# Kernel optimization log

Hardware: AMD Instinct MI355X
Metric: run time of the kernel (lower is better)

The kernel has to match this reference:

```python
import jax, jax.numpy as jnp
import numpy as np

V, T_BLOCK, E, H, L = 65, 256, 384, 6, 10
HS = E // H  # 64


def _ln(x, scale, bias, eps=1e-5):
    mu = jnp.mean(x, axis=-1, keepdims=True)
    var = jnp.mean(jnp.square(x - mu), axis=-1, keepdims=True)
    return (x - mu) * jax.lax.rsqrt(var + eps) * scale + bias


def setup_inputs() -> dict:
    key = jax.random.key(0)
    ks = jax.random.split(key, 20)
    B, T = 64, 256
    s = 0.02
    return {
        "encoding": jax.random.randint(ks[0], (B, T), 0, V),
        "tok_emb": jax.random.normal(ks[1], (V, E), jnp.float32) * s,
        "pos_emb": jax.random.normal(ks[2], (T_BLOCK, E), jnp.float32) * s,
        "Wq": jax.random.normal(ks[3], (L, H, E, HS), jnp.float32) * s,
        "Wk": jax.random.normal(ks[4], (L, H, E, HS), jnp.float32) * s,
        "Wv": jax.random.normal(ks[5], (L, H, E, HS), jnp.float32) * s,
        "Wo": jax.random.normal(ks[6], (L, E, E), jnp.float32) * s,
        "bo": jnp.zeros((L, E), jnp.float32),
        "W1": jax.random.normal(ks[7], (L, E, 4 * E), jnp.float32) * s,
        "b1": jnp.zeros((L, 4 * E), jnp.float32),
        "W2": jax.random.normal(ks[8], (L, 4 * E, E), jnp.float32) * s,
        "b2": jnp.zeros((L, E), jnp.float32),
        "ln1_s": jnp.ones((L, E), jnp.float32),
        "ln1_b": jnp.zeros((L, E), jnp.float32),
        "ln2_s": jnp.ones((L, E), jnp.float32),
        "ln2_b": jnp.zeros((L, E), jnp.float32),
        "lnf_s": jnp.ones((E,), jnp.float32),
        "lnf_b": jnp.zeros((E,), jnp.float32),
        "Wout": jax.random.normal(ks[9], (E, V), jnp.float32) * s,
        "bout": jnp.zeros((V,), jnp.float32),
    }


def reference(encoding, tok_emb, pos_emb, Wq, Wk, Wv, Wo, bo, W1, b1, W2, b2,
              ln1_s, ln1_b, ln2_s, ln2_b, lnf_s, lnf_b, Wout, bout):
    B, T = encoding.shape
    x = tok_emb[encoding] + pos_emb[:T]  # [B,T,E]
    causal = jnp.tril(jnp.ones((T, T), bool))
    scale = jnp.asarray(E, x.dtype) ** -0.5  # NOTE: original scales by embeddingSize, not headSize
    for l in range(L):
        h = _ln(x, ln1_s[l], ln1_b[l])
        q = jnp.einsum('bte,hed->bhtd', h, Wq[l])
        k = jnp.einsum('bte,hed->bhtd', h, Wk[l])
        v = jnp.einsum('bte,hed->bhtd', h, Wv[l])
        scores = jnp.einsum('bhtd,bhsd->bhts', q, k) * scale
        scores = jnp.where(causal, scores, -jnp.inf)
        w = jax.nn.softmax(scores, axis=-1)  # dropout inactive (eval)
        attn = jnp.einsum('bhts,bhsd->bhtd', w, v)  # [B,H,T,HS]
        attn = attn.transpose(0, 2, 1, 3).reshape(B, T, E)  # concat heads
        x = x + attn @ Wo[l] + bo[l]
        h2 = _ln(x, ln2_s[l], ln2_b[l])
        x = x + jax.nn.relu(h2 @ W1[l] + b1[l]) @ W2[l] + b2[l]
    x = _ln(x, lnf_s, lnf_b)
    logits = x @ Wout + bout  # [B,T,V]
    return logits
```

## Files before the change

kernel.cpp:

```cpp
#include <hip/hip_runtime.h>

typedef __bf16 bf16;
typedef __bf16 bf16x4 __attribute__((ext_vector_type(4)));
typedef __bf16 bf16x8 __attribute__((ext_vector_type(8)));
typedef float floatx4 __attribute__((ext_vector_type(4)));

#define NB   64
#define NT   256
#define NE   384
#define NH   6
#define NHS  64
#define NL   10
#define NTOK (NB*NT)
#define NFF  1536
#define NQKV 1152
#define NV   65
#define NVP  128

#define ATTN_SCALE 0.051031036307982884f

__device__ __forceinline__ void glds16(const bf16* g, bf16* l)
{
    __builtin_amdgcn_global_load_lds(
        (const __attribute__((address_space(1))) void*)g,
        (__attribute__((address_space(3))) void*)l, 16, 0, 0);
}

template<int K, int N>
__global__ __launch_bounds__(256) void pack_mat_t(const float* __restrict__ src, bf16* __restrict__ dst)
{
    __shared__ float tile[64][65];
    const int n0 = blockIdx.x * 64, k0 = blockIdx.y * 64, l = blockIdx.z;
    const int tid = threadIdx.x;
    const float* sp = src + (size_t)l * K * N;
#pragma unroll
    for (int it = 0; it < 4; ++it) {
        int kl = (tid >> 4) + it * 16;
        int nl = (tid & 15) * 4;
        float4 v = *(const float4*)(sp + (size_t)(k0 + kl) * N + n0 + nl);
        tile[kl][nl] = v.x; tile[kl][nl + 1] = v.y; tile[kl][nl + 2] = v.z; tile[kl][nl + 3] = v.w;
    }
    __syncthreads();
#pragma unroll
    for (int it = 0; it < 2; ++it) {
        int chunk = it * 256 + tid;
        int nl = chunk >> 3, kc = chunk & 7;
        bf16x8 o;
#pragma unroll
        for (int j = 0; j < 8; ++j) o[j] = (bf16)tile[kc * 8 + j][nl];
        *(bf16x8*)(dst + ((size_t)l * N + n0 + nl) * K + k0 + kc * 8) = o;
    }
}

__global__ __launch_bounds__(256) void pack_qkv_t(const float* __restrict__ Wq, const float* __restrict__ Wk,
                                                  const float* __restrict__ Wv, bf16* __restrict__ dst)
{
    __shared__ float tile[64][65];
    const int n0 = blockIdx.x * 64, k0 = blockIdx.y * 64, l = blockIdx.z;
    const int tid = threadIdx.x;
    const float* src; int hh;
    if (n0 < 384)      { src = Wq; hh = n0 >> 6; }
    else if (n0 < 768) { src = Wk; hh = (n0 - 384) >> 6; }
    else               { src = Wv; hh = (n0 - 768) >> 6; }
    const float* sp = src + ((size_t)l * NH + hh) * NE * NHS;
#pragma unroll
    for (int it = 0; it < 4; ++it) {
        int kl = (tid >> 4) + it * 16;
        int dl = (tid & 15) * 4;
        float4 v = *(const float4*)(sp + (size_t)(k0 + kl) * NHS + dl);
        tile[kl][dl] = v.x; tile[kl][dl + 1] = v.y; tile[kl][dl + 2] = v.z; tile[kl][dl + 3] = v.w;
    }
    __syncthreads();
#pragma unroll
    for (int it = 0; it < 2; ++it) {
        int chunk = it * 256 + tid;
        int nl = chunk >> 3, kc = chunk & 7;
        bf16x8 o;
#pragma unroll
        for (int j = 0; j < 8; ++j) o[j] = (bf16)tile[kc * 8 + j][nl];
        *(bf16x8*)(dst + ((size_t)l * NQKV + n0 + nl) * NE + k0 + kc * 8) = o;
    }
}

__global__ void pack_wout_kernel(const float* __restrict__ Wout, const float* __restrict__ bout,
                                 bf16* __restrict__ dst, float* __restrict__ bias)
{
    int i = blockIdx.x * 256 + threadIdx.x;
    if (i >= NVP * NE) return;
    int k = i % NE, n = i / NE;
    dst[i] = (n < NV) ? (bf16)Wout[(size_t)k * NV + n] : (bf16)0.f;
    if (i < NVP) bias[i] = (i < NV) ? bout[i] : 0.f;
}

__global__ void embed_kernel(const int* __restrict__ enc, const float* __restrict__ tok,
                             const float* __restrict__ pos, float* __restrict__ x)
{
    int i = blockIdx.x * 256 + threadIdx.x;
    if (i >= NTOK * 96) return;
    int row = i / 96, e4 = i % 96;
    int t = row & (NT - 1);
    const float4* tp = (const float4*)(tok + (size_t)enc[row] * NE);
    const float4* pp = (const float4*)(pos + (size_t)t * NE);
    float4 a = tp[e4], p = pp[e4];
    float4 r; r.x = a.x + p.x; r.y = a.y + p.y; r.z = a.z + p.z; r.w = a.w + p.w;
    ((float4*)(x + (size_t)row * NE))[e4] = r;
}

__global__ __launch_bounds__(256) void ln_kernel(const float* __restrict__ xin,
                                                 const float* __restrict__ gam,
                                                 const float* __restrict__ bet,
                                                 bf16* __restrict__ out)
{
    int wave = threadIdx.x >> 6, lane = threadIdx.x & 63;
    size_t row = (size_t)blockIdx.x * 4 + wave;
    const float* xr = xin + row * NE;
    float v[6]; float sum = 0.f;
#pragma unroll
    for (int i = 0; i < 6; ++i) { v[i] = xr[lane + i * 64]; sum += v[i]; }
#pragma unroll
    for (int o = 1; o < 64; o <<= 1) sum += __shfl_xor(sum, o);
    float mu = sum * (1.f / NE);
    float var = 0.f;
#pragma unroll
    for (int i = 0; i < 6; ++i) { float d = v[i] - mu; var += d * d; }
#pragma unroll
    for (int o = 1; o < 64; o <<= 1) var += __shfl_xor(var, o);
    float rs = rsqrtf(var * (1.f / NE) + 1e-5f);
    bf16* orow = out + row * NE;
#pragma unroll
    for (int i = 0; i < 6; ++i) {
        int e = lane + i * 64;
        orow[e] = (bf16)((v[i] - mu) * rs * gam[e] + bet[e]);
    }
}

template<bool BIAS, bool RELU, bool RESID, bool OUTBF16, bool VSPLIT>
__global__ __launch_bounds__(256, 4)
void gemm_kernel(const bf16* __restrict__ A, const bf16* __restrict__ Bt,
                 const float* __restrict__ bias, const float* __restrict__ resid,
                 void* __restrict__ outp, bf16* __restrict__ vt,
                 int M, int K, int out_stride, int n_store)
{
    __shared__ bf16 As[128 * 64];
    __shared__ bf16 Bs[128 * 64];
    const int tid  = threadIdx.x;
    const int wave = tid >> 6;
    const int lane = tid & 63;
    const int quad = lane >> 4;
    const int l16  = lane & 15;
    const int lrow = lane >> 3;
    const int scol = ((lane & 7) ^ lrow) * 8;
    const int m0 = blockIdx.x * 128;
    const int n0 = blockIdx.y * 128;
    const int wm = (wave >> 1) * 64;
    const int wn = (wave & 1) * 64;

    floatx4 acc[4][4];
#pragma unroll
    for (int i = 0; i < 4; ++i)
#pragma unroll
        for (int j = 0; j < 4; ++j) acc[i][j] = (floatx4)0.f;

    const bf16* Ag = A  + (size_t)m0 * K;
    const bf16* Bg = Bt + (size_t)n0 * K;

    for (int k0 = 0; k0 < K; k0 += 64) {
#pragma unroll
        for (int it = 0; it < 4; ++it) {
            int r0 = wave * 32 + it * 8;
            glds16(Ag + (size_t)(r0 + lrow) * K + k0 + scol, &As[r0 * 64]);
            glds16(Bg + (size_t)(r0 + lrow) * K + k0 + scol, &Bs[r0 * 64]);
        }
        __syncthreads();
#pragma unroll
        for (int ko = 0; ko < 2; ++ko) {
            bf16x8 af[4], bfr[4];
#pragma unroll
            for (int mi = 0; mi < 4; ++mi) {
                int r = wm + mi * 16 + l16;
                int c = ((ko * 4 + quad) ^ (r & 7)) * 8;
                af[mi] = *(const bf16x8*)(&As[r * 64 + c]);
            }
#pragma unroll
            for (int ni = 0; ni < 4; ++ni) {
                int r = wn + ni * 16 + l16;
                int c = ((ko * 4 + quad) ^ (r & 7)) * 8;
                bfr[ni] = *(const bf16x8*)(&Bs[r * 64 + c]);
            }
#pragma unroll
            for (int mi = 0; mi < 4; ++mi)
#pragma unroll
                for (int ni = 0; ni < 4; ++ni)
                    acc[mi][ni] = __builtin_amdgcn_mfma_f32_16x16x32_bf16(af[mi], bfr[ni], acc[mi][ni], 0, 0, 0);
        }
        __syncthreads();
    }

#pragma unroll
    for (int mi = 0; mi < 4; ++mi) {
#pragma unroll
        for (int ni = 0; ni < 4; ++ni) {
            int n = n0 + wn + ni * 16 + l16;
            if (VSPLIT && n >= 768) {
                int nn = n - 768;
                int hh = nn >> 6, d = nn & 63;
                int mb = m0 + wm + mi * 16 + quad * 4;
                int bb = mb >> 8, tt = mb & 255;
                bf16x4 pv;
#pragma unroll
                for (int r = 0; r < 4; ++r) pv[r] = (bf16)acc[mi][ni][r];
                *(bf16x4*)(vt + ((size_t)(bb * NH + hh) * NHS + d) * NT + tt) = pv;
                continue;
            }
            float bv = 0.f;
            if (BIAS) bv = bias[n];
#pragma unroll
            for (int r = 0; r < 4; ++r) {
                int m = m0 + wm + mi * 16 + quad * 4 + r;
                float vv = acc[mi][ni][r] + bv;
                if (RELU) vv = fmaxf(vv, 0.f);
                if (n < n_store) {
                    size_t oi = (size_t)m * out_stride + n;
                    if (RESID) vv += resid[oi];
                    if (OUTBF16) ((bf16*)outp)[oi] = (bf16)vv;
                    else         ((float*)outp)[oi] = vv;
                }
            }
        }
    }
}

__global__ __launch_bounds__(256, 3)
void attn_flash_kernel(const bf16* __restrict__ qkv, const bf16* __restrict__ vt,
                       bf16* __restrict__ outp)
{
    __shared__ bf16 Qs[128 * 64];
    __shared__ bf16 Ks[64 * 64];
    __shared__ bf16 Vs[64 * 64];
    __shared__ bf16 Ps[128 * 72];
    const int m0 = blockIdx.x * 128;
    const int z  = blockIdx.y;
    const int b = z / NH, hh = z % NH;
    const int tid = threadIdx.x;
    const int wave = tid >> 6, lane = tid & 63;
    const int quad = lane >> 4, l16 = lane & 15;
    const int lrow = lane >> 3;
    const int scol = ((lane & 7) ^ lrow) * 8;
    const int wm = wave * 32;
    const size_t qbase = (size_t)b * NT * NQKV + hh * NHS;
    const bf16* Vg = vt + (size_t)z * NHS * NT;

#pragma unroll
    for (int it = 0; it < 4; ++it) {
        int r0 = wave * 32 + it * 8;
        glds16(qkv + qbase + (size_t)(m0 + r0 + lrow) * NQKV + scol, &Qs[r0 * 64]);
    }

    floatx4 acc_o[2][4];
    float   psum[2][4];
#pragma unroll
    for (int mi = 0; mi < 2; ++mi) {
#pragma unroll
        for (int ni = 0; ni < 4; ++ni) acc_o[mi][ni] = (floatx4)0.f;
#pragma unroll
        for (int rr = 0; rr < 4; ++rr) psum[mi][rr] = 0.f;
    }

    const int n_ch = (m0 >> 6) + 2;
    for (int ch = 0; ch < n_ch; ++ch) {
        const int s0 = ch * 64;
        {
            int r0 = wave * 16;
            glds16(qkv + qbase + 384 + (size_t)(s0 + r0 + lrow) * NQKV + scol, &Ks[r0 * 64]);
            glds16(qkv + qbase + 384 + (size_t)(s0 + r0 + 8 + lrow) * NQKV + scol, &Ks[(r0 + 8) * 64]);
            glds16(Vg + (size_t)(r0 + lrow) * NT + s0 + scol, &Vs[r0 * 64]);
            glds16(Vg + (size_t)(r0 + 8 + lrow) * NT + s0 + scol, &Vs[(r0 + 8) * 64]);
        }
        __syncthreads();

        floatx4 accs[2][4];
#pragma unroll
        for (int mi = 0; mi < 2; ++mi)
#pragma unroll
            for (int ni = 0; ni < 4; ++ni) accs[mi][ni] = (floatx4)0.f;
#pragma unroll
        for (int ko = 0; ko < 2; ++ko) {
            bf16x8 af[2], bfr[4];
#pragma unroll
            for (int mi = 0; mi < 2; ++mi) {
                int r = wm + mi * 16 + l16;
                af[mi] = *(const bf16x8*)(&Qs[r * 64 + ((ko * 4 + quad) ^ (r & 7)) * 8]);
            }
#pragma unroll
            for (int ni = 0; ni < 4; ++ni) {
                int r = ni * 16 + l16;
                bfr[ni] = *(const bf16x8*)(&Ks[r * 64 + ((ko * 4 + quad) ^ (r & 7)) * 8]);
            }
#pragma unroll
            for (int mi = 0; mi < 2; ++mi)
#pragma unroll
                for (int ni = 0; ni < 4; ++ni)
                    accs[mi][ni] = __builtin_amdgcn_mfma_f32_16x16x32_bf16(af[mi], bfr[ni], accs[mi][ni], 0, 0, 0);
        }

#pragma unroll
        for (int mi = 0; mi < 2; ++mi) {
#pragma unroll
            for (int rr = 0; rr < 4; ++rr) {
                int t = m0 + wm + mi * 16 + quad * 4 + rr;
                float ps = 0.f;
#pragma unroll
                for (int ni = 0; ni < 4; ++ni) {
                    int s = s0 + ni * 16 + l16;
                    float p = (s <= t) ? __expf(accs[mi][ni][rr] * ATTN_SCALE) : 0.f;
                    ps += p;
                    Ps[(wm + mi * 16 + quad * 4 + rr) * 72 + ni * 16 + l16] = (bf16)p;
                }
                psum[mi][rr] += ps;
            }
        }

#pragma unroll
        for (int ko = 0; ko < 2; ++ko) {
            bf16x8 af[2], bfr[4];
#pragma unroll
            for (int mi = 0; mi < 2; ++mi)
                af[mi] = *(const bf16x8*)(&Ps[(wm + mi * 16 + l16) * 72 + ko * 32 + quad * 8]);
#pragma unroll
            for (int ni = 0; ni < 4; ++ni) {
                int r = ni * 16 + l16;
                bfr[ni] = *(const bf16x8*)(&Vs[r * 64 + ((ko * 4 + quad) ^ (r & 7)) * 8]);
            }
#pragma unroll
            for (int mi = 0; mi < 2; ++mi)
#pragma unroll
                for (int ni = 0; ni < 4; ++ni)
                    acc_o[mi][ni] = __builtin_amdgcn_mfma_f32_16x16x32_bf16(af[mi], bfr[ni], acc_o[mi][ni], 0, 0, 0);
        }
        __syncthreads();
    }

#pragma unroll
    for (int mi = 0; mi < 2; ++mi) {
#pragma unroll
        for (int rr = 0; rr < 4; ++rr) {
            float s = psum[mi][rr];
            s += __shfl_xor(s, 1); s += __shfl_xor(s, 2);
            s += __shfl_xor(s, 4); s += __shfl_xor(s, 8);
            psum[mi][rr] = 1.f / s;
        }
    }
#pragma unroll
    for (int mi = 0; mi < 2; ++mi) {
#pragma unroll
        for (int ni = 0; ni < 4; ++ni) {
            int e = hh * NHS + ni * 16 + l16;
#pragma unroll
            for (int rr = 0; rr < 4; ++rr) {
                int m = m0 + wm + mi * 16 + quad * 4 + rr;
                outp[((size_t)b * NT + m) * NE + e] = (bf16)(acc_o[mi][ni][rr] * psum[mi][rr]);
            }
        }
    }
}

extern "C" void kernel_launch(void* const* d_in, const int* in_sizes, int n_in,
                              void* d_out, int out_size, void* d_ws, size_t ws_size,
                              hipStream_t stream)
{
    const int*   enc  = (const int*)d_in[0];
    const float* tok  = (const float*)d_in[1];
    const float* pos  = (const float*)d_in[2];
    const float* Wq   = (const float*)d_in[3];
    const float* Wk   = (const float*)d_in[4];
    const float* Wv   = (const float*)d_in[5];
    const float* Wo   = (const float*)d_in[6];
    const float* bo   = (const float*)d_in[7];
    const float* W1   = (const float*)d_in[8];
    const float* b1   = (const float*)d_in[9];
    const float* W2   = (const float*)d_in[10];
    const float* b2   = (const float*)d_in[11];
    const float* ln1s = (const float*)d_in[12];
    const float* ln1b = (const float*)d_in[13];
    const float* ln2s = (const float*)d_in[14];
    const float* ln2b = (const float*)d_in[15];
    const float* lnfs = (const float*)d_in[16];
    const float* lnfb = (const float*)d_in[17];
    const float* Wout = (const float*)d_in[18];
    const float* bout = (const float*)d_in[19];

    char* ws = (char*)d_ws;
    float* x      = (float*)(ws + 0);
    bf16*  h      = (bf16*)(ws + 25165824);
    bf16*  qkvu   = (bf16*)(ws + 37748736);
    bf16*  attn   = (bf16*)(ws + 88080384);
    bf16*  wqkv   = (bf16*)(ws + 100663296);
    bf16*  wo     = (bf16*)(ws + 109510656);
    bf16*  w1     = (bf16*)(ws + 112459776);
    bf16*  w2     = (bf16*)(ws + 124256256);
    bf16*  wop    = (bf16*)(ws + 136052736);
    float* bop    = (float*)(ws + 136151040);
    bf16*  vt     = (bf16*)(ws + 136151552);

    pack_qkv_t<<<dim3(18, 6, NL), 256, 0, stream>>>(Wq, Wk, Wv, wqkv);
    pack_mat_t<384, 384><<<dim3(6, 6, NL), 256, 0, stream>>>(Wo, wo);
    pack_mat_t<384, 1536><<<dim3(24, 6, NL), 256, 0, stream>>>(W1, w1);
    pack_mat_t<1536, 384><<<dim3(6, 24, NL), 256, 0, stream>>>(W2, w2);
    pack_wout_kernel<<<192, 256, 0, stream>>>(Wout, bout, wop, bop);
    embed_kernel<<<6144, 256, 0, stream>>>(enc, tok, pos, x);

    for (int l = 0; l < NL; ++l) {
        ln_kernel<<<4096, 256, 0, stream>>>(x, ln1s + l * NE, ln1b + l * NE, h);
        gemm_kernel<false, false, false, true, true><<<dim3(128, 9), 256, 0, stream>>>(
            h, wqkv + (size_t)l * NQKV * NE, nullptr, nullptr, qkvu, vt, NTOK, NE, NQKV, NQKV);
        attn_flash_kernel<<<dim3(2, NB * NH), 256, 0, stream>>>(qkvu, vt, attn);
        gemm_kernel<true, false, true, false, false><<<dim3(128, 3), 256, 0, stream>>>(
            attn, wo + (size_t)l * NE * NE, bo + l * NE, x, x, nullptr, NTOK, NE, NE, NE);
        ln_kernel<<<4096, 256, 0, stream>>>(x, ln2s + l * NE, ln2b + l * NE, h);
        gemm_kernel<true, true, false, true, false><<<dim3(128, 12), 256, 0, stream>>>(
            h, w1 + (size_t)l * NFF * NE, b1 + l * NFF, nullptr, qkvu, nullptr, NTOK, NE, NFF, NFF);
        gemm_kernel<true, false, true, false, false><<<dim3(128, 3), 256, 0, stream>>>(
            qkvu, w2 + (size_t)l * NE * NFF, b2 + l * NE, x, x, nullptr, NTOK, NFF, NE, NE);
    }
    ln_kernel<<<4096, 256, 0, stream>>>(x, lnfs, lnfb, h);
    gemm_kernel<true, false, false, false, false><<<dim3(128, 1), 256, 0, stream>>>(
        h, wop, bop, nullptr, d_out, nullptr, NTOK, NE, NV, NV);
}
```

Before: 1.522 ms.

## Store residual stream in bf16 and use 64-row tiles for narrow GEMMs

The residual activation x changes from fp32 to bf16 in the embed, layernorm and residual-add GEMM epilogues, which halves the traffic for the residual stream. The GEMM is templated on the M tile size, and the N=384 projections (Wo, W2, output head) now use 64-row tiles so the grid is twice as large. Layernorm is vectorised with bf16x4 and float4 loads. Accumulating the residual in bf16 over 10 layers costs accuracy and may drift from the fp32 reference.

```diff
diff --git a/kernel.cpp b/kernel.cpp
--- a/kernel.cpp
+++ b/kernel.cpp
@@ -93,7 +93,7 @@
 }
 
 __global__ void embed_kernel(const int* __restrict__ enc, const float* __restrict__ tok,
-                             const float* __restrict__ pos, float* __restrict__ x)
+                             const float* __restrict__ pos, bf16* __restrict__ x)
 {
     int i = blockIdx.x * 256 + threadIdx.x;
     if (i >= NTOK * 96) return;
@@ -102,46 +102,70 @@
     const float4* tp = (const float4*)(tok + (size_t)enc[row] * NE);
     const float4* pp = (const float4*)(pos + (size_t)t * NE);
     float4 a = tp[e4], p = pp[e4];
-    float4 r; r.x = a.x + p.x; r.y = a.y + p.y; r.z = a.z + p.z; r.w = a.w + p.w;
-    ((float4*)(x + (size_t)row * NE))[e4] = r;
-}
-
-__global__ __launch_bounds__(256) void ln_kernel(const float* __restrict__ xin,
+    bf16x4 r;
+    r[0] = (bf16)(a.x + p.x); r[1] = (bf16)(a.y + p.y);
+    r[2] = (bf16)(a.z + p.z); r[3] = (bf16)(a.w + p.w);
+    *(bf16x4*)(x + (size_t)row * NE + e4 * 4) = r;
+}
+
+__global__ __launch_bounds__(256) void ln_kernel(const bf16* __restrict__ xin,
                                                  const float* __restrict__ gam,
                                                  const float* __restrict__ bet,
                                                  bf16* __restrict__ out)
 {
     int wave = threadIdx.x >> 6, lane = threadIdx.x & 63;
     size_t row = (size_t)blockIdx.x * 4 + wave;
-    const float* xr = xin + row * NE;
-    float v[6]; float sum = 0.f;
-#pragma unroll
-    for (int i = 0; i < 6; ++i) { v[i] = xr[lane + i * 64]; sum += v[i]; }
+    const bf16x4* xr = (const bf16x4*)(xin + row * NE);
+    bf16x4 c0 = xr[lane];
+    bf16x4 c1 = (lane < 32) ? xr[64 + lane] : (bf16x4)(bf16)0.f;
+    float v[8]; float sum = 0.f;
+#pragma unroll
+    for (int j = 0; j < 4; ++j) { v[j] = (float)c0[j]; sum += v[j]; }
+#pragma unroll
+    for (int j = 0; j < 4; ++j) { v[4 + j] = (float)c1[j]; sum += v[4 + j]; }
 #pragma unroll
     for (int o = 1; o < 64; o <<= 1) sum += __shfl_xor(sum, o);
     float mu = sum * (1.f / NE);
     float var = 0.f;
 #pragma unroll
-    for (int i = 0; i < 6; ++i) { float d = v[i] - mu; var += d * d; }
+    for (int j = 0; j < 4; ++j) { float d = v[j] - mu; var += d * d; }
+    if (lane < 32) {
+#pragma unroll
+        for (int j = 0; j < 4; ++j) { float d = v[4 + j] - mu; var += d * d; }
+    }
 #pragma unroll
     for (int o = 1; o < 64; o <<= 1) var += __shfl_xor(var, o);
     float rs = rsqrtf(var * (1.f / NE) + 1e-5f);
-    bf16* orow = out + row * NE;
-#pragma unroll
-    for (int i = 0; i < 6; ++i) {
-        int e = lane + i * 64;
-        orow[e] = (bf16)((v[i] - mu) * rs * gam[e] + bet[e]);
-    }
-}
-
-template<bool BIAS, bool RELU, bool RESID, bool OUTBF16, bool VSPLIT>
+    bf16x4* orow = (bf16x4*)(out + row * NE);
+    {
+        float4 g = ((const float4*)gam)[lane], bb = ((const float4*)bet)[lane];
+        bf16x4 o4;
+        o4[0] = (bf16)((v[0] - mu) * rs * g.x + bb.x);
+        o4[1] = (bf16)((v[1] - mu) * rs * g.y + bb.y);
+        o4[2] = (bf16)((v[2] - mu) * rs * g.z + bb.z);
+        o4[3] = (bf16)((v[3] - mu) * rs * g.w + bb.w);
+        orow[lane] = o4;
+    }
+    if (lane < 32) {
+        float4 g = ((const float4*)gam)[64 + lane], bb = ((const float4*)bet)[64 + lane];
+        bf16x4 o4;
+        o4[0] = (bf16)((v[4] - mu) * rs * g.x + bb.x);
+        o4[1] = (bf16)((v[5] - mu) * rs * g.y + bb.y);
+        o4[2] = (bf16)((v[6] - mu) * rs * g.z + bb.z);
+        o4[3] = (bf16)((v[7] - mu) * rs * g.w + bb.w);
+        orow[64 + lane] = o4;
+    }
+}
+
+template<int MT, bool BIAS, bool RELU, bool RESID, bool OUTBF16, bool VSPLIT>
 __global__ __launch_bounds__(256, 4)
 void gemm_kernel(const bf16* __restrict__ A, const bf16* __restrict__ Bt,
-                 const float* __restrict__ bias, const float* __restrict__ resid,
+                 const float* __restrict__ bias, const bf16* __restrict__ resid,
                  void* __restrict__ outp, bf16* __restrict__ vt,
                  int M, int K, int out_stride, int n_store)
 {
-    __shared__ bf16 As[128 * 64];
+    constexpr int MI = MT / 32;
+    __shared__ bf16 As[MT * 64];
     __shared__ bf16 Bs[128 * 64];
     const int tid  = threadIdx.x;
     const int wave = tid >> 6;
@@ -150,14 +174,14 @@
     const int l16  = lane & 15;
     const int lrow = lane >> 3;
     const int scol = ((lane & 7) ^ lrow) * 8;
-    const int m0 = blockIdx.x * 128;
+    const int m0 = blockIdx.x * MT;
     const int n0 = blockIdx.y * 128;
-    const int wm = (wave >> 1) * 64;
+    const int wm = (wave >> 1) * (MT / 2);
     const int wn = (wave & 1) * 64;
 
-    floatx4 acc[4][4];
-#pragma unroll
-    for (int i = 0; i < 4; ++i)
+    floatx4 acc[MI][4];
+#pragma unroll
+    for (int i = 0; i < MI; ++i)
 #pragma unroll
         for (int j = 0; j < 4; ++j) acc[i][j] = (floatx4)0.f;
 
@@ -166,17 +190,21 @@
 
     for (int k0 = 0; k0 < K; k0 += 64) {
 #pragma unroll
+        for (int it = 0; it < MT / 32; ++it) {
+            int r0 = wave * (MT / 4) + it * 8;
+            glds16(Ag + (size_t)(r0 + lrow) * K + k0 + scol, &As[r0 * 64]);
+        }
+#pragma unroll
         for (int it = 0; it < 4; ++it) {
             int r0 = wave * 32 + it * 8;
-            glds16(Ag + (size_t)(r0 + lrow) * K + k0 + scol, &As[r0 * 64]);
             glds16(Bg + (size_t)(r0 + lrow) * K + k0 + scol, &Bs[r0 * 64]);
         }
         __syncthreads();
 #pragma unroll
         for (int ko = 0; ko < 2; ++ko) {
-            bf16x8 af[4], bfr[4];
-#pragma unroll
-            for (int mi = 0; mi < 4; ++mi) {
+            bf16x8 af[MI], bfr[4];
+#pragma unroll
+            for (int mi = 0; mi < MI; ++mi) {
                 int r = wm + mi * 16 + l16;
                 int c = ((ko * 4 + quad) ^ (r & 7)) * 8;
                 af[mi] = *(const bf16x8*)(&As[r * 64 + c]);
@@ -188,7 +216,7 @@
                 bfr[ni] = *(const bf16x8*)(&Bs[r * 64 + c]);
             }
 #pragma unroll
-            for (int mi = 0; mi < 4; ++mi)
+            for (int mi = 0; mi < MI; ++mi)
 #pragma unroll
                 for (int ni = 0; ni < 4; ++ni)
                     acc[mi][ni] = __builtin_amdgcn_mfma_f32_16x16x32_bf16(af[mi], bfr[ni], acc[mi][ni], 0, 0, 0);
@@ -197,7 +225,7 @@
     }
 
 #pragma unroll
-    for (int mi = 0; mi < 4; ++mi) {
+    for (int mi = 0; mi < MI; ++mi) {
 #pragma unroll
         for (int ni = 0; ni < 4; ++ni) {
             int n = n0 + wn + ni * 16 + l16;
@@ -221,7 +249,7 @@
                 if (RELU) vv = fmaxf(vv, 0.f);
                 if (n < n_store) {
                     size_t oi = (size_t)m * out_stride + n;
-                    if (RESID) vv += resid[oi];
+                    if (RESID) vv += (float)resid[oi];
                     if (OUTBF16) ((bf16*)outp)[oi] = (bf16)vv;
                     else         ((float*)outp)[oi] = vv;
                 }
@@ -390,17 +418,17 @@
     const float* bout = (const float*)d_in[19];
 
     char* ws = (char*)d_ws;
-    float* x      = (float*)(ws + 0);
-    bf16*  h      = (bf16*)(ws + 25165824);
-    bf16*  qkvu   = (bf16*)(ws + 37748736);
-    bf16*  attn   = (bf16*)(ws + 88080384);
-    bf16*  wqkv   = (bf16*)(ws + 100663296);
-    bf16*  wo     = (bf16*)(ws + 109510656);
-    bf16*  w1     = (bf16*)(ws + 112459776);
-    bf16*  w2     = (bf16*)(ws + 124256256);
-    bf16*  wop    = (bf16*)(ws + 136052736);
-    float* bop    = (float*)(ws + 136151040);
-    bf16*  vt     = (bf16*)(ws + 136151552);
+    bf16*  x      = (bf16*)(ws + 0);
+    bf16*  h      = (bf16*)(ws + 12582912);
+    bf16*  qkvu   = (bf16*)(ws + 25165824);
+    bf16*  attn   = (bf16*)(ws + 75497472);
+    bf16*  wqkv   = (bf16*)(ws + 88080384);
+    bf16*  wo     = (bf16*)(ws + 96927744);
+    bf16*  w1     = (bf16*)(ws + 99876864);
+    bf16*  w2     = (bf16*)(ws + 111673344);
+    bf16*  wop    = (bf16*)(ws + 123469824);
+    float* bop    = (float*)(ws + 123568128);
+    bf16*  vt     = (bf16*)(ws + 123568640);
 
     pack_qkv_t<<<dim3(18, 6, NL), 256, 0, stream>>>(Wq, Wk, Wv, wqkv);
     pack_mat_t<384, 384><<<dim3(6, 6, NL), 256, 0, stream>>>(Wo, wo);
@@ -411,18 +439,18 @@
 
     for (int l = 0; l < NL; ++l) {
         ln_kernel<<<4096, 256, 0, stream>>>(x, ln1s + l * NE, ln1b + l * NE, h);
-        gemm_kernel<false, false, false, true, true><<<dim3(128, 9), 256, 0, stream>>>(
+        gemm_kernel<128, false, false, false, true, true><<<dim3(128, 9), 256, 0, stream>>>(
             h, wqkv + (size_t)l * NQKV * NE, nullptr, nullptr, qkvu, vt, NTOK, NE, NQKV, NQKV);
         attn_flash_kernel<<<dim3(2, NB * NH), 256, 0, stream>>>(qkvu, vt, attn);
-        gemm_kernel<true, false, true, false, false><<<dim3(128, 3), 256, 0, stream>>>(
+        gemm_kernel<64, true, false, true, true, false><<<dim3(256, 3), 256, 0, stream>>>(
             attn, wo + (size_t)l * NE * NE, bo + l * NE, x, x, nullptr, NTOK, NE, NE, NE);
         ln_kernel<<<4096, 256, 0, stream>>>(x, ln2s + l * NE, ln2b + l * NE, h);
-        gemm_kernel<true, true, false, true, false><<<dim3(128, 12), 256, 0, stream>>>(
+        gemm_kernel<128, true, true, false, true, false><<<dim3(128, 12), 256, 0, stream>>>(
             h, w1 + (size_t)l * NFF * NE, b1 + l * NFF, nullptr, qkvu, nullptr, NTOK, NE, NFF, NFF);
-        gemm_kernel<true, false, true, false, false><<<dim3(128, 3), 256, 0, stream>>>(
+        gemm_kernel<64, true, false, true, true, false><<<dim3(256, 3), 256, 0, stream>>>(
             qkvu, w2 + (size_t)l * NE * NFF, b2 + l * NE, x, x, nullptr, NTOK, NFF, NE, NE);
     }
     ln_kernel<<<4096, 256, 0, stream>>>(x, lnfs, lnfb, h);
-    gemm_kernel<true, false, false, false, false><<<dim3(128, 1), 256, 0, stream>>>(
+    gemm_kernel<64, true, false, false, false, false><<<dim3(256, 1), 256, 0, stream>>>(
         h, wop, bop, nullptr, d_out, nullptr, NTOK, NE, NV, NV);
 }
```

Result: faster. 1.417 ms (-6.9%).
